# Performance work log

Hardware: AMD Instinct MI355X
Metric: run time of the kernel (lower is better)

The kernel has to match this reference:

```python
import jax, jax.numpy as jnp
import numpy as np

B, S, D, H, F, E, K = 2, 2048, 1024, 16, 4096, 8, 2
DK = D // H


def _ln(x, g, b, eps=1e-5):
    m = jnp.mean(x, axis=-1, keepdims=True)
    v = jnp.var(x, axis=-1, keepdims=True)
    return (x - m) * jax.lax.rsqrt(v + eps) * g + b


def _silu(x):
    return x * jax.nn.sigmoid(x)


def _gated_proj(x, w1, b1, w2, b2):
    # SiLU(x W1 + b1) * (x W2 + b2)
    return _silu(x @ w1 + b1) * (x @ w2 + b2)


def setup_inputs() -> dict:
    key = jax.random.key(0)
    ks = jax.random.split(key, 32)

    def n(k, shape, s=0.02):
        return jax.random.normal(k, shape, jnp.float32) * s

    inp = {
        "x": jax.random.normal(ks[0], (B, S, D), jnp.float32),
        "wq1": n(ks[1], (D, D)), "bq1": jnp.zeros((D,), jnp.float32),
        "wq2": n(ks[2], (D, D)), "bq2": jnp.zeros((D,), jnp.float32),
        "wk1": n(ks[3], (D, D)), "bk1": jnp.zeros((D,), jnp.float32),
        "wk2": n(ks[4], (D, D)), "bk2": jnp.zeros((D,), jnp.float32),
        "wv1": n(ks[5], (D, D)), "bv1": jnp.zeros((D,), jnp.float32),
        "wv2": n(ks[6], (D, D)), "bv2": jnp.zeros((D,), jnp.float32),
        "wo": n(ks[7], (D, D)), "bo": jnp.zeros((D,), jnp.float32),
        "ln1_g": jnp.ones((D,), jnp.float32), "ln1_b": jnp.zeros((D,), jnp.float32),
        "ln2_g": jnp.ones((D,), jnp.float32), "ln2_b": jnp.zeros((D,), jnp.float32),
        "gate_w": n(ks[8], (D, E)), "gate_b": jnp.zeros((E,), jnp.float32),
        "e_w1": n(ks[9], (E, D, F)), "e_b1": jnp.zeros((E, F), jnp.float32),
        "e_w2": n(ks[10], (E, F, D)), "e_b2": jnp.zeros((E, D), jnp.float32),
        "e_w3": n(ks[11], (E, D, F)), "e_b3": jnp.zeros((E, F), jnp.float32),
    }
    return inp


def _attention(x2, wq1, bq1, wq2, bq2, wk1, bk1, wk2, bk2,
               wv1, bv1, wv2, bv2, wo, bo, eps=1e-6):
    q = _gated_proj(x2, wq1, bq1, wq2, bq2).reshape(B, S, H, DK)
    k = _gated_proj(x2, wk1, bk1, wk2, bk2).reshape(B, S, H, DK)
    v = _gated_proj(x2, wv1, bv1, wv2, bv2).reshape(B, S, H, DK)
    phi_q = jax.nn.elu(q) + 1.0
    phi_k = jax.nn.elu(k) + 1.0
    # kv: [B,H,DK,DK] -- associative reordering of linear attention
    kv = jnp.einsum("bshd,bshe->bhde", phi_k, v)
    ksum = jnp.sum(phi_k, axis=1)  # [B,H,DK]
    qksum = jnp.einsum("bshd,bhd->bsh", phi_q, ksum)
    num = jnp.einsum("bshd,bhde->bshe", phi_q, kv)
    out = num / (qksum[..., None] + eps)  # [B,S,H,DK]
    return out.reshape(B, S, D) @ wo + bo


def _moe(x2, gate_w, gate_b, e_w1, e_b1, e_w2, e_b2, e_w3, e_b3):
    gate_probs = jax.nn.softmax(x2 @ gate_w + gate_b, axis=-1)  # [B,S,E]
    topv, topi = jax.lax.top_k(gate_probs, K)  # [B,S,K]
    topv = topv / (jnp.sum(topv, axis=-1, keepdims=True) + 1e-6)
    # combine weight per expert: [B,S,E]
    comb = jnp.sum(jax.nn.one_hot(topi, E, dtype=x2.dtype) * topv[..., None], axis=-2)
    out = jnp.zeros_like(x2)
    for e in range(E):  # small fixed expert count
        h = _silu(x2 @ e_w1[e] + e_b1[e]) * (x2 @ e_w3[e] + e_b3[e])
        out = out + (h @ e_w2[e] + e_b2[e]) * comb[..., e, None]
    return out


def reference(x, wq1, bq1, wq2, bq2, wk1, bk1, wk2, bk2, wv1, bv1, wv2, bv2,
              wo, bo, ln1_g, ln1_b, ln2_g, ln2_b, gate_w, gate_b,
              e_w1, e_b1, e_w2, e_b2, e_w3, e_b3):
    x2 = _ln(x, ln1_g, ln1_b)
    x = x + _attention(x2, wq1, bq1, wq2, bq2, wk1, bk1, wk2, bk2,
                       wv1, bv1, wv2, bv2, wo, bo)
    x2 = _ln(x, ln2_g, ln2_b)
    x = x + _moe(x2, gate_w, gate_b, e_w1, e_b1, e_w2, e_b2, e_w3, e_b3)
    return x
```

## Files before the change

kernel.cpp:

```cpp
#include <hip/hip_runtime.h>
#include <cstdint>
#include <cstddef>

typedef __bf16 bf16;
typedef bf16  bf16x8 __attribute__((ext_vector_type(8)));
typedef bf16  bf16x4 __attribute__((ext_vector_type(4)));
typedef float f32x4  __attribute__((ext_vector_type(4)));

#define B_ 2
#define S_ 2048
#define D_ 1024
#define H_ 16
#define F_ 4096
#define E_ 8
#define T_ (B_*S_)

__device__ __forceinline__ void gl16(const bf16* g, bf16* l) {
    __builtin_amdgcn_global_load_lds(
        (const __attribute__((address_space(1))) void*)g,
        (__attribute__((address_space(3))) void*)l, 16, 0, 0);
}

__global__ __launch_bounds__(256) void transpose_convert(const float* __restrict__ in,
                                                         bf16* __restrict__ out,
                                                         int R, int C) {
    __shared__ float tile[32][33];
    size_t mat = blockIdx.z;
    in  += mat * (size_t)R * C;
    out += mat * (size_t)R * C;
    int c0 = blockIdx.x * 32, r0 = blockIdx.y * 32;
    for (int i = threadIdx.y; i < 32; i += 8)
        tile[i][threadIdx.x] = in[(size_t)(r0 + i) * C + c0 + threadIdx.x];
    __syncthreads();
    for (int i = threadIdx.y; i < 32; i += 8)
        out[(size_t)(c0 + i) * R + r0 + threadIdx.x] = (bf16)tile[threadIdx.x][i];
}

__global__ __launch_bounds__(256) void ln_kernel(const float* __restrict__ xin,
                                                 const float* __restrict__ gam,
                                                 const float* __restrict__ bet,
                                                 bf16* __restrict__ obf,
                                                 float* __restrict__ of32) {
    int row = blockIdx.x, tid = threadIdx.x;
    const float4* xr = (const float4*)(xin + (size_t)row * D_);
    float4 v = xr[tid];
    float s  = v.x + v.y + v.z + v.w;
    float s2 = v.x*v.x + v.y*v.y + v.z*v.z + v.w*v.w;
    #pragma unroll
    for (int o = 1; o < 64; o <<= 1) { s += __shfl_xor(s, o); s2 += __shfl_xor(s2, o); }
    __shared__ float red[8];
    int wave = tid >> 6, lane = tid & 63;
    if (lane == 0) { red[wave] = s; red[4 + wave] = s2; }
    __syncthreads();
    s  = red[0] + red[1] + red[2] + red[3];
    s2 = red[4] + red[5] + red[6] + red[7];
    float m   = s * (1.0f / D_);
    float var = s2 * (1.0f / D_) - m * m;
    float rs  = rsqrtf(var + 1e-5f);
    float4 gv = ((const float4*)gam)[tid];
    float4 bv = ((const float4*)bet)[tid];
    float y0 = (v.x - m) * rs * gv.x + bv.x;
    float y1 = (v.y - m) * rs * gv.y + bv.y;
    float y2 = (v.z - m) * rs * gv.z + bv.z;
    float y3 = (v.w - m) * rs * gv.w + bv.w;
    bf16x4 ov; ov[0] = (bf16)y0; ov[1] = (bf16)y1; ov[2] = (bf16)y2; ov[3] = (bf16)y3;
    *(bf16x4*)(obf + (size_t)row * D_ + tid * 4) = ov;
    if (of32) {
        float4 o4; o4.x = y0; o4.y = y1; o4.z = y2; o4.w = y3;
        ((float4*)of32)[(size_t)row * (D_/4) + tid] = o4;
    }
}


template<int MODE>
__global__ __launch_bounds__(256) void gemm_dual128(const bf16* __restrict__ A,
                                                    const bf16* __restrict__ B1,
                                                    const bf16* __restrict__ B2,
                                                    const float* __restrict__ bias1,
                                                    const float* __restrict__ bias2,
                                                    float* __restrict__ out,
                                                    int N, int K) {
    __shared__ alignas(16) bf16 As [2][128 * 32];
    __shared__ alignas(16) bf16 B1s[2][64 * 32];
    __shared__ alignas(16) bf16 B2s[2][64 * 32];
    const int tid = threadIdx.x;
    const int wave = tid >> 6, lane = tid & 63;
    const int nb = blockIdx.x, mb = blockIdx.y;
    const int wr = (wave >> 1) * 64;
    const int wc = (wave & 1) * 32;
    const int fr = lane & 15, fk = (lane >> 4) * 8;
    const int srow = lane >> 2, scol = (lane & 3) * 8;
    const int co = wave * 512;
    const bf16* Ap0 = A  + (size_t)(mb * 128 + wave * 16 + srow) * K + scol;
    const bf16* Ap1 = A  + (size_t)(mb * 128 + (wave + 4) * 16 + srow) * K + scol;
    const bf16* B1p = B1 + (size_t)(nb * 64 + wave * 16 + srow) * K + scol;
    const bf16* B2p = B2 + (size_t)(nb * 64 + wave * 16 + srow) * K + scol;
    f32x4 acc1[4][2] = {};
    f32x4 acc2[4][2] = {};
    gl16(Ap0, &As[0][co]);
    gl16(Ap1, &As[0][co + 2048]);
    gl16(B1p, &B1s[0][co]);
    gl16(B2p, &B2s[0][co]);
    __syncthreads();
    int cur = 0;
    for (int k0 = 32; k0 < K; k0 += 32) {
        int nxt = cur ^ 1;
        gl16(Ap0 + k0, &As[nxt][co]);
        gl16(Ap1 + k0, &As[nxt][co + 2048]);
        gl16(B1p + k0, &B1s[nxt][co]);
        gl16(B2p + k0, &B2s[nxt][co]);
        bf16x8 af[4];
        #pragma unroll
        for (int mi = 0; mi < 4; mi++)
            af[mi] = *(const bf16x8*)&As[cur][(wr + mi * 16 + fr) * 32 + fk];
        #pragma unroll
        for (int ni = 0; ni < 2; ni++) {
            bf16x8 b1f = *(const bf16x8*)&B1s[cur][(wc + ni * 16 + fr) * 32 + fk];
            bf16x8 b2f = *(const bf16x8*)&B2s[cur][(wc + ni * 16 + fr) * 32 + fk];
            #pragma unroll
            for (int mi = 0; mi < 4; mi++) {
                acc1[mi][ni] = __builtin_amdgcn_mfma_f32_16x16x32_bf16(af[mi], b1f, acc1[mi][ni], 0, 0, 0);
                acc2[mi][ni] = __builtin_amdgcn_mfma_f32_16x16x32_bf16(af[mi], b2f, acc2[mi][ni], 0, 0, 0);
            }
        }
        __syncthreads();
        cur = nxt;
    }
    {
        bf16x8 af[4];
        #pragma unroll
        for (int mi = 0; mi < 4; mi++)
            af[mi] = *(const bf16x8*)&As[cur][(wr + mi * 16 + fr) * 32 + fk];
        #pragma unroll
        for (int ni = 0; ni < 2; ni++) {
            bf16x8 b1f = *(const bf16x8*)&B1s[cur][(wc + ni * 16 + fr) * 32 + fk];
            bf16x8 b2f = *(const bf16x8*)&B2s[cur][(wc + ni * 16 + fr) * 32 + fk];
            #pragma unroll
            for (int mi = 0; mi < 4; mi++) {
                acc1[mi][ni] = __builtin_amdgcn_mfma_f32_16x16x32_bf16(af[mi], b1f, acc1[mi][ni], 0, 0, 0);
                acc2[mi][ni] = __builtin_amdgcn_mfma_f32_16x16x32_bf16(af[mi], b2f, acc2[mi][ni], 0, 0, 0);
            }
        }
    }
    const int col = lane & 15, rowq = (lane >> 4) * 4;
    #pragma unroll
    for (int ni = 0; ni < 2; ni++) {
        int gn = nb * 64 + wc + ni * 16 + col;
        float bb1 = bias1[gn], bb2 = bias2[gn];
        #pragma unroll
        for (int mi = 0; mi < 4; mi++) {
            #pragma unroll
            for (int r = 0; r < 4; r++) {
                int gm = mb * 128 + wr + mi * 16 + rowq + r;
                float p1 = acc1[mi][ni][r] + bb1;
                float p2 = acc2[mi][ni][r] + bb2;
                float g = (p1 / (1.0f + expf(-p1))) * p2;
                size_t idx = (size_t)gm * N + gn;
                if (MODE == 0) {
                    float e = g > 0.0f ? g : expm1f(g);
                    out[idx] = e + 1.0f;
                } else {
                    out[idx] = g;
                }
            }
        }
    }
}

__global__ __launch_bounds__(256) void gemm_single128(const bf16* __restrict__ A,
                                                      const bf16* __restrict__ Bt,
                                                      float* __restrict__ out,
                                                      int N, int K) {
    __shared__ alignas(16) bf16 As[2][128 * 32];
    __shared__ alignas(16) bf16 Bs[2][128 * 32];
    const int tid = threadIdx.x;
    const int wave = tid >> 6, lane = tid & 63;
    const int nb = blockIdx.x, mb = blockIdx.y;
    const int wr = (wave >> 1) * 64, wc = (wave & 1) * 64;
    const int fr = lane & 15, fk = (lane >> 4) * 8;
    const int srow = lane >> 2, scol = (lane & 3) * 8;
    const int co = wave * 512;
    const bf16* Ap0 = A  + (size_t)(mb * 128 + wave * 16 + srow) * K + scol;
    const bf16* Ap1 = A  + (size_t)(mb * 128 + (wave + 4) * 16 + srow) * K + scol;
    const bf16* Bp0 = Bt + (size_t)(nb * 128 + wave * 16 + srow) * K + scol;
    const bf16* Bp1 = Bt + (size_t)(nb * 128 + (wave + 4) * 16 + srow) * K + scol;
    f32x4 acc[4][4] = {};
    gl16(Ap0, &As[0][co]);
    gl16(Ap1, &As[0][co + 2048]);
    gl16(Bp0, &Bs[0][co]);
    gl16(Bp1, &Bs[0][co + 2048]);
    __syncthreads();
    int cur = 0;
    for (int k0 = 32; k0 < K; k0 += 32) {
        int nxt = cur ^ 1;
        gl16(Ap0 + k0, &As[nxt][co]);
        gl16(Ap1 + k0, &As[nxt][co + 2048]);
        gl16(Bp0 + k0, &Bs[nxt][co]);
        gl16(Bp1 + k0, &Bs[nxt][co + 2048]);
        bf16x8 af[4], bf[4];
        #pragma unroll
        for (int mi = 0; mi < 4; mi++)
            af[mi] = *(const bf16x8*)&As[cur][(wr + mi * 16 + fr) * 32 + fk];
        #pragma unroll
        for (int ni = 0; ni < 4; ni++)
            bf[ni] = *(const bf16x8*)&Bs[cur][(wc + ni * 16 + fr) * 32 + fk];
        #pragma unroll
        for (int ni = 0; ni < 4; ni++)
            #pragma unroll
            for (int mi = 0; mi < 4; mi++)
                acc[mi][ni] = __builtin_amdgcn_mfma_f32_16x16x32_bf16(af[mi], bf[ni], acc[mi][ni], 0, 0, 0);
        __syncthreads();
        cur = nxt;
    }
    {
        bf16x8 af[4], bf[4];
        #pragma unroll
        for (int mi = 0; mi < 4; mi++)
            af[mi] = *(const bf16x8*)&As[cur][(wr + mi * 16 + fr) * 32 + fk];
        #pragma unroll
        for (int ni = 0; ni < 4; ni++)
            bf[ni] = *(const bf16x8*)&Bs[cur][(wc + ni * 16 + fr) * 32 + fk];
        #pragma unroll
        for (int ni = 0; ni < 4; ni++)
            #pragma unroll
            for (int mi = 0; mi < 4; mi++)
                acc[mi][ni] = __builtin_amdgcn_mfma_f32_16x16x32_bf16(af[mi], bf[ni], acc[mi][ni], 0, 0, 0);
    }
    const int col = lane & 15, rowq = (lane >> 4) * 4;
    #pragma unroll
    for (int ni = 0; ni < 4; ni++) {
        int gn = nb * 128 + wc + ni * 16 + col;
        #pragma unroll
        for (int mi = 0; mi < 4; mi++)
            #pragma unroll
            for (int r = 0; r < 4; r++) {
                int gm = mb * 128 + wr + mi * 16 + rowq + r;
                out[(size_t)gm * N + gn] = acc[mi][ni][r];
            }
    }
}

__global__ __launch_bounds__(256) void gemm_dual_moe128(const bf16* __restrict__ A,
                                                        const bf16* __restrict__ B1all,
                                                        const bf16* __restrict__ B2all,
                                                        const float* __restrict__ b1all,
                                                        const float* __restrict__ b2all,
                                                        const int* __restrict__ list,
                                                        const int* __restrict__ counts,
                                                        const int* __restrict__ ebase,
                                                        bf16* __restrict__ outAct,
                                                        int N, int K) {
    const int e = blockIdx.z;
    const int cnt = counts[e * 64];
    const int mb = blockIdx.y;
    if (mb * 128 >= cnt) return;
    __shared__ alignas(16) bf16 As [2][128 * 32];
    __shared__ alignas(16) bf16 B1s[2][64 * 32];
    __shared__ alignas(16) bf16 B2s[2][64 * 32];
    const bf16* B1 = B1all + (size_t)e * N * K;
    const bf16* B2 = B2all + (size_t)e * N * K;
    const float* bias1 = b1all + (size_t)e * N;
    const float* bias2 = b2all + (size_t)e * N;
    const int tid = threadIdx.x;
    const int wave = tid >> 6, lane = tid & 63;
    const int nb = blockIdx.x;
    const int wr = (wave >> 1) * 64, wc = (wave & 1) * 32;
    const int fr = lane & 15, fk = (lane >> 4) * 8;
    const int srow = lane >> 2, scol = (lane & 3) * 8;
    const int co = wave * 512;
    int gr0 = mb * 128 + wave * 16 + srow;
    int gr1 = mb * 128 + (wave + 4) * 16 + srow;
    int tok0 = list[e * T_ + (gr0 < cnt ? gr0 : cnt - 1)];
    int tok1 = list[e * T_ + (gr1 < cnt ? gr1 : cnt - 1)];
    const bf16* Ap0 = A  + (size_t)tok0 * K + scol;
    const bf16* Ap1 = A  + (size_t)tok1 * K + scol;
    const bf16* B1p = B1 + (size_t)(nb * 64 + wave * 16 + srow) * K + scol;
    const bf16* B2p = B2 + (size_t)(nb * 64 + wave * 16 + srow) * K + scol;
    f32x4 acc1[4][2] = {};
    f32x4 acc2[4][2] = {};
    gl16(Ap0, &As[0][co]);
    gl16(Ap1, &As[0][co + 2048]);
    gl16(B1p, &B1s[0][co]);
    gl16(B2p, &B2s[0][co]);
    __syncthreads();
    int cur = 0;
    for (int k0 = 32; k0 < K; k0 += 32) {
        int nxt = cur ^ 1;
        gl16(Ap0 + k0, &As[nxt][co]);
        gl16(Ap1 + k0, &As[nxt][co + 2048]);
        gl16(B1p + k0, &B1s[nxt][co]);
        gl16(B2p + k0, &B2s[nxt][co]);
        bf16x8 af[4];
        #pragma unroll
        for (int mi = 0; mi < 4; mi++)
            af[mi] = *(const bf16x8*)&As[cur][(wr + mi * 16 + fr) * 32 + fk];
        #pragma unroll
        for (int ni = 0; ni < 2; ni++) {
            bf16x8 b1f = *(const bf16x8*)&B1s[cur][(wc + ni * 16 + fr) * 32 + fk];
            bf16x8 b2f = *(const bf16x8*)&B2s[cur][(wc + ni * 16 + fr) * 32 + fk];
            #pragma unroll
            for (int mi = 0; mi < 4; mi++) {
                acc1[mi][ni] = __builtin_amdgcn_mfma_f32_16x16x32_bf16(af[mi], b1f, acc1[mi][ni], 0, 0, 0);
                acc2[mi][ni] = __builtin_amdgcn_mfma_f32_16x16x32_bf16(af[mi], b2f, acc2[mi][ni], 0, 0, 0);
            }
        }
        __syncthreads();
        cur = nxt;
    }
    {
        bf16x8 af[4];
        #pragma unroll
        for (int mi = 0; mi < 4; mi++)
            af[mi] = *(const bf16x8*)&As[cur][(wr + mi * 16 + fr) * 32 + fk];
        #pragma unroll
        for (int ni = 0; ni < 2; ni++) {
            bf16x8 b1f = *(const bf16x8*)&B1s[cur][(wc + ni * 16 + fr) * 32 + fk];
            bf16x8 b2f = *(const bf16x8*)&B2s[cur][(wc + ni * 16 + fr) * 32 + fk];
            #pragma unroll
            for (int mi = 0; mi < 4; mi++) {
                acc1[mi][ni] = __builtin_amdgcn_mfma_f32_16x16x32_bf16(af[mi], b1f, acc1[mi][ni], 0, 0, 0);
                acc2[mi][ni] = __builtin_amdgcn_mfma_f32_16x16x32_bf16(af[mi], b2f, acc2[mi][ni], 0, 0, 0);
            }
        }
    }
    const int col = lane & 15, rowq = (lane >> 4) * 4;
    const size_t rbase = (size_t)ebase[e] + mb * 128;
    #pragma unroll
    for (int ni = 0; ni < 2; ni++) {
        int gn = nb * 64 + wc + ni * 16 + col;
        float bb1 = bias1[gn], bb2 = bias2[gn];
        #pragma unroll
        for (int mi = 0; mi < 4; mi++)
            #pragma unroll
            for (int r = 0; r < 4; r++) {
                int lm = wr + mi * 16 + rowq + r;
                float p1 = acc1[mi][ni][r] + bb1;
                float p2 = acc2[mi][ni][r] + bb2;
                float g = (p1 / (1.0f + expf(-p1))) * p2;
                outAct[(rbase + lm) * N + gn] = (bf16)g;
            }
    }
}

__global__ __launch_bounds__(256) void gemm_down_moe128(const bf16* __restrict__ Act,
                                                        const bf16* __restrict__ Ball,
                                                        const float* __restrict__ ball,
                                                        const int* __restrict__ list,
                                                        const float* __restrict__ wgt,
                                                        const int* __restrict__ counts,
                                                        const int* __restrict__ ebase,
                                                        float* __restrict__ out,
                                                        int N, int K) {
    const int e = blockIdx.z;
    const int cnt = counts[e * 64];
    const int mb = blockIdx.y;
    if (mb * 128 >= cnt) return;
    __shared__ alignas(16) bf16 As[2][128 * 32];
    __shared__ alignas(16) bf16 Bs[2][128 * 32];
    const bf16* A  = Act + (size_t)ebase[e] * K;
    const bf16* Bt = Ball + (size_t)e * N * K;
    const float* bias = ball + (size_t)e * N;
    const int tid = threadIdx.x;
    const int wave = tid >> 6, lane = tid & 63;
    const int nb = blockIdx.x;
    const int wr = (wave >> 1) * 64, wc = (wave & 1) * 64;
    const int fr = lane & 15, fk = (lane >> 4) * 8;
    const int srow = lane >> 2, scol = (lane & 3) * 8;
    const int co = wave * 512;
    const bf16* Ap0 = A  + (size_t)(mb * 128 + wave * 16 + srow) * K + scol;
    const bf16* Ap1 = A  + (size_t)(mb * 128 + (wave + 4) * 16 + srow) * K + scol;
    const bf16* Bp0 = Bt + (size_t)(nb * 128 + wave * 16 + srow) * K + scol;
    const bf16* Bp1 = Bt + (size_t)(nb * 128 + (wave + 4) * 16 + srow) * K + scol;
    f32x4 acc[4][4] = {};
    gl16(Ap0, &As[0][co]);
    gl16(Ap1, &As[0][co + 2048]);
    gl16(Bp0, &Bs[0][co]);
    gl16(Bp1, &Bs[0][co + 2048]);
    __syncthreads();
    int cur = 0;
    for (int k0 = 32; k0 < K; k0 += 32) {
        int nxt = cur ^ 1;
        gl16(Ap0 + k0, &As[nxt][co]);
        gl16(Ap1 + k0, &As[nxt][co + 2048]);
        gl16(Bp0 + k0, &Bs[nxt][co]);
        gl16(Bp1 + k0, &Bs[nxt][co + 2048]);
        bf16x8 af[4], bf[4];
        #pragma unroll
        for (int mi = 0; mi < 4; mi++)
            af[mi] = *(const bf16x8*)&As[cur][(wr + mi * 16 + fr) * 32 + fk];
        #pragma unroll
        for (int ni = 0; ni < 4; ni++)
            bf[ni] = *(const bf16x8*)&Bs[cur][(wc + ni * 16 + fr) * 32 + fk];
        #pragma unroll
        for (int ni = 0; ni < 4; ni++)
            #pragma unroll
            for (int mi = 0; mi < 4; mi++)
                acc[mi][ni] = __builtin_amdgcn_mfma_f32_16x16x32_bf16(af[mi], bf[ni], acc[mi][ni], 0, 0, 0);
        __syncthreads();
        cur = nxt;
    }
    {
        bf16x8 af[4], bf[4];
        #pragma unroll
        for (int mi = 0; mi < 4; mi++)
            af[mi] = *(const bf16x8*)&As[cur][(wr + mi * 16 + fr) * 32 + fk];
        #pragma unroll
        for (int ni = 0; ni < 4; ni++)
            bf[ni] = *(const bf16x8*)&Bs[cur][(wc + ni * 16 + fr) * 32 + fk];
        #pragma unroll
        for (int ni = 0; ni < 4; ni++)
            #pragma unroll
            for (int mi = 0; mi < 4; mi++)
                acc[mi][ni] = __builtin_amdgcn_mfma_f32_16x16x32_bf16(af[mi], bf[ni], acc[mi][ni], 0, 0, 0);
    }
    const int col = lane & 15, rowq = (lane >> 4) * 4;
    #pragma unroll
    for (int ni = 0; ni < 4; ni++) {
        int gn = nb * 128 + wc + ni * 16 + col;
        float bb = bias[gn];
        #pragma unroll
        for (int mi = 0; mi < 4; mi++)
            #pragma unroll
            for (int r = 0; r < 4; r++) {
                int gm = mb * 128 + wr + mi * 16 + rowq + r;
                if (gm < cnt) {
                    int tok = list[e * T_ + gm];
                    float w = wgt[e * T_ + gm];
                    atomicAdd(&out[(size_t)tok * N + gn], (acc[mi][ni][r] + bb) * w);
                }
            }
    }
}

__global__ __launch_bounds__(256) void attn_kv_part(const float* __restrict__ phi_k,
                                                    const float* __restrict__ vv_g,
                                                    float* __restrict__ kvp,
                                                    float* __restrict__ ksp) {
    int bh = blockIdx.x;
    int chunk = blockIdx.y;
    int b = bh >> 4, h = bh & 15;
    __shared__ float pk[64][68];
    __shared__ float vv[64][68];
    int tid = threadIdx.x;
    int d0 = (tid >> 4) * 4;
    int e0 = (tid & 15) * 4;
    float acc[4][4] = {};
    float ks[4] = {};
    int sbeg = chunk * (S_ / 8);
    for (int s0 = sbeg; s0 < sbeg + S_ / 8; s0 += 64) {
        __syncthreads();
        for (int i = tid; i < 1024; i += 256) {
            int r = i >> 4, c4 = i & 15;
            size_t base = ((size_t)(b * S_ + s0 + r) * D_ + h * 64);
            ((float4*)&pk[r][0])[c4] = ((const float4*)(phi_k + base))[c4];
            ((float4*)&vv[r][0])[c4] = ((const float4*)(vv_g + base))[c4];
        }
        __syncthreads();
        for (int s = 0; s < 64; s++) {
            float a0 = pk[s][d0], a1 = pk[s][d0+1], a2 = pk[s][d0+2], a3 = pk[s][d0+3];
            float b0 = vv[s][e0], b1 = vv[s][e0+1], b2 = vv[s][e0+2], b3 = vv[s][e0+3];
            acc[0][0] += a0*b0; acc[0][1] += a0*b1; acc[0][2] += a0*b2; acc[0][3] += a0*b3;
            acc[1][0] += a1*b0; acc[1][1] += a1*b1; acc[1][2] += a1*b2; acc[1][3] += a1*b3;
            acc[2][0] += a2*b0; acc[2][1] += a2*b1; acc[2][2] += a2*b2; acc[2][3] += a2*b3;
            acc[3][0] += a3*b0; acc[3][1] += a3*b1; acc[3][2] += a3*b2; acc[3][3] += a3*b3;
            if ((tid & 15) == 0) { ks[0] += a0; ks[1] += a1; ks[2] += a2; ks[3] += a3; }
        }
    }
    float* kvo = kvp + ((size_t)bh * 8 + chunk) * 4096;
    for (int i = 0; i < 4; i++)
        for (int j = 0; j < 4; j++)
            kvo[(d0 + i) * 64 + e0 + j] = acc[i][j];
    if ((tid & 15) == 0)
        for (int i = 0; i < 4; i++) ksp[((size_t)bh * 8 + chunk) * 64 + d0 + i] = ks[i];
}

__global__ __launch_bounds__(256) void attn_kv_reduce(const float* __restrict__ kvp,
                                                      const float* __restrict__ ksp,
                                                      float* __restrict__ kv,
                                                      float* __restrict__ ksum) {
    int bh = blockIdx.x;
    int tid = threadIdx.x;
    #pragma unroll
    for (int i = 0; i < 4; i++) {
        int idx = i * 256 + tid;
        float4 s = {0, 0, 0, 0};
        #pragma unroll
        for (int c = 0; c < 8; c++) {
            float4 p = ((const float4*)(kvp + ((size_t)bh * 8 + c) * 4096))[idx];
            s.x += p.x; s.y += p.y; s.z += p.z; s.w += p.w;
        }
        ((float4*)(kv + (size_t)bh * 4096))[idx] = s;
    }
    if (tid < 64) {
        float s = 0;
        #pragma unroll
        for (int c = 0; c < 8; c++) s += ksp[((size_t)bh * 8 + c) * 64 + tid];
        ksum[bh * 64 + tid] = s;
    }
}

__global__ __launch_bounds__(256) void attn_num(const float* __restrict__ phi_q,
                                                const float* __restrict__ kv,
                                                const float* __restrict__ ksum,
                                                bf16* __restrict__ outb) {
    int bh = blockIdx.y;
    int b = bh >> 4, h = bh & 15;
    int s0 = blockIdx.x * 64;
    __shared__ float kvs[64][64];
    __shared__ float pqs[64][68];
    __shared__ float kss[64];
    int tid = threadIdx.x;
    const float* kvsrc = kv + (size_t)bh * 4096;
    for (int i = tid; i < 1024; i += 256) ((float4*)kvs)[i] = ((const float4*)kvsrc)[i];
    if (tid < 16) ((float4*)kss)[tid] = ((const float4*)(ksum + bh * 64))[tid];
    for (int i = tid; i < 1024; i += 256) {
        int r = i >> 4, c4 = i & 15;
        ((float4*)&pqs[r][0])[c4] =
            ((const float4*)(phi_q + ((size_t)(b * S_ + s0 + r) * D_ + h * 64)))[c4];
    }
    __syncthreads();
    int tok = tid >> 2;
    int e0  = (tid & 3) * 16;
    float acc[16] = {};
    float qk = 0.0f;
    for (int d = 0; d < 64; d++) {
        float pq = pqs[tok][d];
        qk += pq * kss[d];
        #pragma unroll
        for (int ei = 0; ei < 16; ei++) acc[ei] += pq * kvs[d][e0 + ei];
    }
    float inv = 1.0f / (qk + 1e-6f);
    int t = b * S_ + s0 + tok;
    bf16* op = outb + (size_t)t * D_ + h * 64 + e0;
    #pragma unroll
    for (int ei = 0; ei < 16; ei++) op[ei] = (bf16)(acc[ei] * inv);
}

__global__ __launch_bounds__(256) void residual_kernel(const float* __restrict__ x,
                                                       const float* __restrict__ prod,
                                                       const float* __restrict__ bo,
                                                       float* __restrict__ x1,
                                                       float* __restrict__ outp) {
    int i = blockIdx.x * 256 + threadIdx.x;
    float4 xv = ((const float4*)x)[i];
    float4 pv = ((const float4*)prod)[i];
    float4 bv = ((const float4*)bo)[i & 255];
    float4 r;
    r.x = xv.x + pv.x + bv.x; r.y = xv.y + pv.y + bv.y;
    r.z = xv.z + pv.z + bv.z; r.w = xv.w + pv.w + bv.w;
    ((float4*)x1)[i] = r;
    ((float4*)outp)[i] = r;
}

__global__ void zero_counts(int* counts) {
    counts[threadIdx.x] = 0;
}

__global__ void expert_bases(const int* __restrict__ counts, int* __restrict__ ebase) {
    if (threadIdx.x == 0) {
        int b = 0;
        #pragma unroll
        for (int e = 0; e < E_; e++) {
            ebase[e] = b;
            b += (counts[e * 64] + 127) & ~127;
        }
    }
}

__global__ __launch_bounds__(256) void gate_kernel(const float* __restrict__ x2f,
                                                   const float* __restrict__ gw,
                                                   const float* __restrict__ gb,
                                                   int* __restrict__ counts,
                                                   int* __restrict__ list,
                                                   float* __restrict__ wgt) {
    int tid = threadIdx.x;
    int wave = tid >> 6, lane = tid & 63;
    int t = blockIdx.x * 4 + wave;
    const float* xr = x2f + (size_t)t * D_;
    float le[8] = {};
    for (int i = 0; i < 16; i++) {
        int d = lane + i * 64;
        float xv = xr[d];
        const float4* g4 = (const float4*)(gw + (size_t)d * 8);
        float4 a = g4[0], b = g4[1];
        le[0] += xv * a.x; le[1] += xv * a.y; le[2] += xv * a.z; le[3] += xv * a.w;
        le[4] += xv * b.x; le[5] += xv * b.y; le[6] += xv * b.z; le[7] += xv * b.w;
    }
    #pragma unroll
    for (int o = 1; o < 64; o <<= 1)
        #pragma unroll
        for (int e = 0; e < 8; e++) le[e] += __shfl_xor(le[e], o);
    if (lane == 0) {
        float probs[8]; float mx = -1e30f;
        for (int e = 0; e < 8; e++) { le[e] += gb[e]; mx = fmaxf(mx, le[e]); }
        float s = 0.0f;
        for (int e = 0; e < 8; e++) { probs[e] = expf(le[e] - mx); s += probs[e]; }
        float invs = 1.0f / s;
        for (int e = 0; e < 8; e++) probs[e] *= invs;
        int i1 = 0; float v1 = probs[0];
        for (int e = 1; e < 8; e++) if (probs[e] > v1) { v1 = probs[e]; i1 = e; }
        int i2 = -1; float v2 = -1.0f;
        for (int e = 0; e < 8; e++) if (e != i1 && probs[e] > v2) { v2 = probs[e]; i2 = e; }
        float inv = 1.0f / (v1 + v2 + 1e-6f);
        int p1 = atomicAdd(&counts[i1 * 64], 1);
        list[i1 * T_ + p1] = t; wgt[i1 * T_ + p1] = v1 * inv;
        int p2 = atomicAdd(&counts[i2 * 64], 1);
        list[i2 * T_ + p2] = t; wgt[i2 * T_ + p2] = v2 * inv;
    }
}

extern "C" void kernel_launch(void* const* d_in, const int* in_sizes, int n_in,
                              void* d_out, int out_size, void* d_ws, size_t ws_size,
                              hipStream_t stream) {
    const float* x    = (const float*)d_in[0];
    const float* wq1  = (const float*)d_in[1];
    const float* bq1  = (const float*)d_in[2];
    const float* wq2  = (const float*)d_in[3];
    const float* bq2  = (const float*)d_in[4];
    const float* wk1  = (const float*)d_in[5];
    const float* bk1  = (const float*)d_in[6];
    const float* wk2  = (const float*)d_in[7];
    const float* bk2  = (const float*)d_in[8];
    const float* wv1  = (const float*)d_in[9];
    const float* bv1  = (const float*)d_in[10];
    const float* wv2  = (const float*)d_in[11];
    const float* bv2  = (const float*)d_in[12];
    const float* wo   = (const float*)d_in[13];
    const float* bo   = (const float*)d_in[14];
    const float* ln1g = (const float*)d_in[15];
    const float* ln1b = (const float*)d_in[16];
    const float* ln2g = (const float*)d_in[17];
    const float* ln2b = (const float*)d_in[18];
    const float* gw   = (const float*)d_in[19];
    const float* gb   = (const float*)d_in[20];
    const float* ew1  = (const float*)d_in[21];
    const float* eb1  = (const float*)d_in[22];
    const float* ew2  = (const float*)d_in[23];
    const float* eb2  = (const float*)d_in[24];
    const float* ew3  = (const float*)d_in[25];
    const float* eb3  = (const float*)d_in[26];
    float* out = (float*)d_out;

    char* wsb = (char*)d_ws;
    size_t off = 0;
    auto carve = [&](size_t bytes) -> char* {
        char* r = wsb + off;
        off = (off + bytes + 255) & ~(size_t)255;
        return r;
    };
    bf16* Wq1t = (bf16*)carve((size_t)D_ * D_ * 2);
    bf16* Wq2t = (bf16*)carve((size_t)D_ * D_ * 2);
    bf16* Wk1t = (bf16*)carve((size_t)D_ * D_ * 2);
    bf16* Wk2t = (bf16*)carve((size_t)D_ * D_ * 2);
    bf16* Wv1t = (bf16*)carve((size_t)D_ * D_ * 2);
    bf16* Wv2t = (bf16*)carve((size_t)D_ * D_ * 2);
    bf16* Wot  = (bf16*)carve((size_t)D_ * D_ * 2);
    bf16* We1t = (bf16*)carve((size_t)E_ * D_ * F_ * 2);
    bf16* We3t = (bf16*)carve((size_t)E_ * D_ * F_ * 2);
    bf16* We2t = (bf16*)carve((size_t)E_ * D_ * F_ * 2);
    bf16*  X2b  = (bf16*)carve((size_t)T_ * D_ * 2);
    float* PhiQ = (float*)carve((size_t)T_ * D_ * 4);
    float* PhiK = (float*)carve((size_t)T_ * D_ * 4);
    float* Vb   = (float*)carve((size_t)T_ * D_ * 4);
    float* KV   = (float*)carve((size_t)B_ * H_ * 64 * 64 * 4);
    float* KS   = (float*)carve((size_t)B_ * H_ * 64 * 4);
    float* KVp  = (float*)carve((size_t)B_ * H_ * 8 * 64 * 64 * 4);
    float* KSp  = (float*)carve((size_t)B_ * H_ * 8 * 64 * 4);
    bf16*  Attn = (bf16*)carve((size_t)T_ * D_ * 2);
    float* WoP  = (float*)carve((size_t)T_ * D_ * 4);
    float* X1   = (float*)carve((size_t)T_ * D_ * 4);
    bf16*  X2c  = (bf16*)carve((size_t)T_ * D_ * 2);
    int*   Cnt  = (int*)carve((size_t)E_ * 64 * 4);
    int*   List = (int*)carve((size_t)E_ * T_ * 4);
    float* Wgt  = (float*)carve((size_t)E_ * T_ * 4);
    int*   Ebase = (int*)carve((size_t)E_ * 4);
    bf16*  Act  = (bf16*)PhiQ;
    float* X2f  = WoP;

    dim3 tb32(32, 8);
    transpose_convert<<<dim3(32, 32, 1), tb32, 0, stream>>>(wq1, Wq1t, D_, D_);
    transpose_convert<<<dim3(32, 32, 1), tb32, 0, stream>>>(wq2, Wq2t, D_, D_);
    transpose_convert<<<dim3(32, 32, 1), tb32, 0, stream>>>(wk1, Wk1t, D_, D_);
    transpose_convert<<<dim3(32, 32, 1), tb32, 0, stream>>>(wk2, Wk2t, D_, D_);
    transpose_convert<<<dim3(32, 32, 1), tb32, 0, stream>>>(wv1, Wv1t, D_, D_);
    transpose_convert<<<dim3(32, 32, 1), tb32, 0, stream>>>(wv2, Wv2t, D_, D_);
    transpose_convert<<<dim3(32, 32, 1), tb32, 0, stream>>>(wo,  Wot,  D_, D_);
    transpose_convert<<<dim3(F_/32, D_/32, E_), tb32, 0, stream>>>(ew1, We1t, D_, F_);
    transpose_convert<<<dim3(F_/32, D_/32, E_), tb32, 0, stream>>>(ew3, We3t, D_, F_);
    transpose_convert<<<dim3(D_/32, F_/32, E_), tb32, 0, stream>>>(ew2, We2t, F_, D_);

    zero_counts<<<1, E_ * 64, 0, stream>>>(Cnt);

    ln_kernel<<<T_, 256, 0, stream>>>(x, ln1g, ln1b, X2b, nullptr);

    gemm_dual128<0><<<dim3(D_/64, T_/128), 256, 0, stream>>>(X2b, Wq1t, Wq2t, bq1, bq2, PhiQ, D_, D_);
    gemm_dual128<0><<<dim3(D_/64, T_/128), 256, 0, stream>>>(X2b, Wk1t, Wk2t, bk1, bk2, PhiK, D_, D_);
    gemm_dual128<1><<<dim3(D_/64, T_/128), 256, 0, stream>>>(X2b, Wv1t, Wv2t, bv1, bv2, Vb,   D_, D_);

    attn_kv_part<<<dim3(B_ * H_, 8), 256, 0, stream>>>(PhiK, Vb, KVp, KSp);
    attn_kv_reduce<<<B_ * H_, 256, 0, stream>>>(KVp, KSp, KV, KS);
    attn_num<<<dim3(S_/64, B_ * H_), 256, 0, stream>>>(PhiQ, KV, KS, Attn);

    gemm_single128<<<dim3(D_/128, T_/128), 256, 0, stream>>>(Attn, Wot, WoP, D_, D_);
    residual_kernel<<<T_ * D_ / 1024, 256, 0, stream>>>(x, WoP, bo, X1, out);

    ln_kernel<<<T_, 256, 0, stream>>>(X1, ln2g, ln2b, X2c, X2f);
    gate_kernel<<<T_ / 4, 256, 0, stream>>>(X2f, gw, gb, Cnt, List, Wgt);
    expert_bases<<<1, 64, 0, stream>>>(Cnt, Ebase);

    gemm_dual_moe128<<<dim3(F_/64, T_/128, E_), 256, 0, stream>>>(
        X2c, We1t, We3t, eb1, eb3, List, Cnt, Ebase, Act, F_, D_);
    gemm_down_moe128<<<dim3(D_/128, T_/128, E_), 256, 0, stream>>>(
        Act, We2t, eb2, List, Wgt, Cnt, Ebase, out, D_, F_);
}
```

Baseline: 1.159 ms.

## Triple-buffer GEMM K-loop with explicit waitcnt; vectorize weight transpose with swizzled LDS

All four GEMM kernels switch from double to triple-buffered LDS staging. Loads run two k-tiles ahead, and the full __syncthreads is replaced by s_waitcnt vmcnt(4) plus s_barrier, so global-to-LDS loads overlap more with MFMA work. The weight transpose/convert kernel now handles 256x64 tiles, reading with float4 and writing bf16x8 through an XOR-swizzled bf16 LDS buffer, which cuts per-element transactions. In exchange, LDS use per GEMM block rises by half, which may reduce occupancy, and the vmcnt counts must match exactly the four loads issued per stage.

```diff
diff --git a/kernel.cpp b/kernel.cpp
--- a/kernel.cpp
+++ b/kernel.cpp
@@ -24,16 +24,29 @@
 __global__ __launch_bounds__(256) void transpose_convert(const float* __restrict__ in,
                                                          bf16* __restrict__ out,
                                                          int R, int C) {
-    __shared__ float tile[32][33];
+    __shared__ bf16 tbuf[64 * 256];
     size_t mat = blockIdx.z;
     in  += mat * (size_t)R * C;
     out += mat * (size_t)R * C;
-    int c0 = blockIdx.x * 32, r0 = blockIdx.y * 32;
-    for (int i = threadIdx.y; i < 32; i += 8)
-        tile[i][threadIdx.x] = in[(size_t)(r0 + i) * C + c0 + threadIdx.x];
+    int c0 = blockIdx.x * 64, r0 = blockIdx.y * 256;
+    for (int i = threadIdx.x; i < 256 * 16; i += 256) {
+        int row = i >> 4, cb = (i & 15) * 4;
+        float4 v = *(const float4*)(in + (size_t)(r0 + row) * C + c0 + cb);
+        float vv[4] = {v.x, v.y, v.z, v.w};
+        #pragma unroll
+        for (int k = 0; k < 4; k++) {
+            int c = cb + k;
+            int key = ((c >> 2) & 7) << 3;
+            tbuf[c * 256 + (row ^ key)] = (bf16)vv[k];
+        }
+    }
     __syncthreads();
-    for (int i = threadIdx.y; i < 32; i += 8)
-        out[(size_t)(c0 + i) * R + r0 + threadIdx.x] = (bf16)tile[threadIdx.x][i];
+    for (int i = threadIdx.x; i < 64 * 32; i += 256) {
+        int c = i >> 5, r8 = (i & 31) * 8;
+        int key = ((c >> 2) & 7) << 3;
+        *(bf16x8*)(out + (size_t)(c0 + c) * R + r0 + r8) =
+            *(const bf16x8*)&tbuf[c * 256 + (r8 ^ key)];
+    }
 }
 
 __global__ __launch_bounds__(256) void ln_kernel(const float* __restrict__ xin,
@@ -80,14 +93,13 @@
                                                     const float* __restrict__ bias2,
                                                     float* __restrict__ out,
                                                     int N, int K) {
-    __shared__ alignas(16) bf16 As [2][128 * 32];
-    __shared__ alignas(16) bf16 B1s[2][64 * 32];
-    __shared__ alignas(16) bf16 B2s[2][64 * 32];
+    __shared__ alignas(16) bf16 As [3][128 * 32];
+    __shared__ alignas(16) bf16 B1s[3][64 * 32];
+    __shared__ alignas(16) bf16 B2s[3][64 * 32];
     const int tid = threadIdx.x;
     const int wave = tid >> 6, lane = tid & 63;
     const int nb = blockIdx.x, mb = blockIdx.y;
-    const int wr = (wave >> 1) * 64;
-    const int wc = (wave & 1) * 32;
+    const int wr = (wave >> 1) * 64, wc = (wave & 1) * 32;
     const int fr = lane & 15, fk = (lane >> 4) * 8;
     const int srow = lane >> 2, scol = (lane & 3) * 8;
     const int co = wave * 512;
@@ -97,51 +109,39 @@
     const bf16* B2p = B2 + (size_t)(nb * 64 + wave * 16 + srow) * K + scol;
     f32x4 acc1[4][2] = {};
     f32x4 acc2[4][2] = {};
-    gl16(Ap0, &As[0][co]);
-    gl16(Ap1, &As[0][co + 2048]);
-    gl16(B1p, &B1s[0][co]);
-    gl16(B2p, &B2s[0][co]);
-    __syncthreads();
-    int cur = 0;
-    for (int k0 = 32; k0 < K; k0 += 32) {
-        int nxt = cur ^ 1;
-        gl16(Ap0 + k0, &As[nxt][co]);
-        gl16(Ap1 + k0, &As[nxt][co + 2048]);
-        gl16(B1p + k0, &B1s[nxt][co]);
-        gl16(B2p + k0, &B2s[nxt][co]);
+    const int NT = K >> 5;
+#define STG_DU(t_, s_) { int k0_ = (t_) << 5; \
+        gl16(Ap0 + k0_, &As[s_][co]); \
+        gl16(Ap1 + k0_, &As[s_][co + 2048]); \
+        gl16(B1p + k0_, &B1s[s_][co]); \
+        gl16(B2p + k0_, &B2s[s_][co]); }
+    STG_DU(0, 0); STG_DU(1, 1);
+    asm volatile("s_waitcnt vmcnt(4)" ::: "memory");
+    __builtin_amdgcn_s_barrier();
+    for (int t = 0; t < NT; ++t) {
+        int s = t % 3;
+        if (t + 2 < NT) STG_DU(t + 2, (t + 2) % 3);
         bf16x8 af[4];
         #pragma unroll
         for (int mi = 0; mi < 4; mi++)
-            af[mi] = *(const bf16x8*)&As[cur][(wr + mi * 16 + fr) * 32 + fk];
+            af[mi] = *(const bf16x8*)&As[s][(wr + mi * 16 + fr) * 32 + fk];
         #pragma unroll
         for (int ni = 0; ni < 2; ni++) {
-            bf16x8 b1f = *(const bf16x8*)&B1s[cur][(wc + ni * 16 + fr) * 32 + fk];
-            bf16x8 b2f = *(const bf16x8*)&B2s[cur][(wc + ni * 16 + fr) * 32 + fk];
+            bf16x8 b1f = *(const bf16x8*)&B1s[s][(wc + ni * 16 + fr) * 32 + fk];
+            bf16x8 b2f = *(const bf16x8*)&B2s[s][(wc + ni * 16 + fr) * 32 + fk];
             #pragma unroll
             for (int mi = 0; mi < 4; mi++) {
                 acc1[mi][ni] = __builtin_amdgcn_mfma_f32_16x16x32_bf16(af[mi], b1f, acc1[mi][ni], 0, 0, 0);
                 acc2[mi][ni] = __builtin_amdgcn_mfma_f32_16x16x32_bf16(af[mi], b2f, acc2[mi][ni], 0, 0, 0);
             }
         }
-        __syncthreads();
-        cur = nxt;
-    }
-    {
-        bf16x8 af[4];
-        #pragma unroll
-        for (int mi = 0; mi < 4; mi++)
-            af[mi] = *(const bf16x8*)&As[cur][(wr + mi * 16 + fr) * 32 + fk];
-        #pragma unroll
-        for (int ni = 0; ni < 2; ni++) {
-            bf16x8 b1f = *(const bf16x8*)&B1s[cur][(wc + ni * 16 + fr) * 32 + fk];
-            bf16x8 b2f = *(const bf16x8*)&B2s[cur][(wc + ni * 16 + fr) * 32 + fk];
-            #pragma unroll
-            for (int mi = 0; mi < 4; mi++) {
-                acc1[mi][ni] = __builtin_amdgcn_mfma_f32_16x16x32_bf16(af[mi], b1f, acc1[mi][ni], 0, 0, 0);
-                acc2[mi][ni] = __builtin_amdgcn_mfma_f32_16x16x32_bf16(af[mi], b2f, acc2[mi][ni], 0, 0, 0);
-            }
-        }
-    }
+        if (t + 1 < NT) {
+            if (t + 2 < NT) asm volatile("s_waitcnt vmcnt(4) lgkmcnt(0)" ::: "memory");
+            else            asm volatile("s_waitcnt vmcnt(0) lgkmcnt(0)" ::: "memory");
+            __builtin_amdgcn_s_barrier();
+        }
+    }
+#undef STG_DU
     const int col = lane & 15, rowq = (lane >> 4) * 4;
     #pragma unroll
     for (int ni = 0; ni < 2; ni++) {
@@ -171,8 +171,8 @@
                                                       const bf16* __restrict__ Bt,
                                                       float* __restrict__ out,
                                                       int N, int K) {
-    __shared__ alignas(16) bf16 As[2][128 * 32];
-    __shared__ alignas(16) bf16 Bs[2][128 * 32];
+    __shared__ alignas(16) bf16 As[3][128 * 32];
+    __shared__ alignas(16) bf16 Bs[3][128 * 32];
     const int tid = threadIdx.x;
     const int wave = tid >> 6, lane = tid & 63;
     const int nb = blockIdx.x, mb = blockIdx.y;
@@ -185,47 +185,37 @@
     const bf16* Bp0 = Bt + (size_t)(nb * 128 + wave * 16 + srow) * K + scol;
     const bf16* Bp1 = Bt + (size_t)(nb * 128 + (wave + 4) * 16 + srow) * K + scol;
     f32x4 acc[4][4] = {};
-    gl16(Ap0, &As[0][co]);
-    gl16(Ap1, &As[0][co + 2048]);
-    gl16(Bp0, &Bs[0][co]);
-    gl16(Bp1, &Bs[0][co + 2048]);
-    __syncthreads();
-    int cur = 0;
-    for (int k0 = 32; k0 < K; k0 += 32) {
-        int nxt = cur ^ 1;
-        gl16(Ap0 + k0, &As[nxt][co]);
-        gl16(Ap1 + k0, &As[nxt][co + 2048]);
-        gl16(Bp0 + k0, &Bs[nxt][co]);
-        gl16(Bp1 + k0, &Bs[nxt][co + 2048]);
+    const int NT = K >> 5;
+#define STG_SG(t_, s_) { int k0_ = (t_) << 5; \
+        gl16(Ap0 + k0_, &As[s_][co]); \
+        gl16(Ap1 + k0_, &As[s_][co + 2048]); \
+        gl16(Bp0 + k0_, &Bs[s_][co]); \
+        gl16(Bp1 + k0_, &Bs[s_][co + 2048]); }
+    STG_SG(0, 0); STG_SG(1, 1);
+    asm volatile("s_waitcnt vmcnt(4)" ::: "memory");
+    __builtin_amdgcn_s_barrier();
+    for (int t = 0; t < NT; ++t) {
+        int s = t % 3;
+        if (t + 2 < NT) STG_SG(t + 2, (t + 2) % 3);
         bf16x8 af[4], bf[4];
         #pragma unroll
         for (int mi = 0; mi < 4; mi++)
-            af[mi] = *(const bf16x8*)&As[cur][(wr + mi * 16 + fr) * 32 + fk];
+            af[mi] = *(const bf16x8*)&As[s][(wr + mi * 16 + fr) * 32 + fk];
         #pragma unroll
         for (int ni = 0; ni < 4; ni++)
-            bf[ni] = *(const bf16x8*)&Bs[cur][(wc + ni * 16 + fr) * 32 + fk];
+            bf[ni] = *(const bf16x8*)&Bs[s][(wc + ni * 16 + fr) * 32 + fk];
         #pragma unroll
         for (int ni = 0; ni < 4; ni++)
             #pragma unroll
             for (int mi = 0; mi < 4; mi++)
                 acc[mi][ni] = __builtin_amdgcn_mfma_f32_16x16x32_bf16(af[mi], bf[ni], acc[mi][ni], 0, 0, 0);
-        __syncthreads();
-        cur = nxt;
-    }
-    {
-        bf16x8 af[4], bf[4];
-        #pragma unroll
-        for (int mi = 0; mi < 4; mi++)
-            af[mi] = *(const bf16x8*)&As[cur][(wr + mi * 16 + fr) * 32 + fk];
-        #pragma unroll
-        for (int ni = 0; ni < 4; ni++)
-            bf[ni] = *(const bf16x8*)&Bs[cur][(wc + ni * 16 + fr) * 32 + fk];
-        #pragma unroll
-        for (int ni = 0; ni < 4; ni++)
-            #pragma unroll
-            for (int mi = 0; mi < 4; mi++)
-                acc[mi][ni] = __builtin_amdgcn_mfma_f32_16x16x32_bf16(af[mi], bf[ni], acc[mi][ni], 0, 0, 0);
-    }
+        if (t + 1 < NT) {
+            if (t + 2 < NT) asm volatile("s_waitcnt vmcnt(4) lgkmcnt(0)" ::: "memory");
+            else            asm volatile("s_waitcnt vmcnt(0) lgkmcnt(0)" ::: "memory");
+            __builtin_amdgcn_s_barrier();
+        }
+    }
+#undef STG_SG
     const int col = lane & 15, rowq = (lane >> 4) * 4;
     #pragma unroll
     for (int ni = 0; ni < 4; ni++) {
@@ -254,9 +244,9 @@
     const int cnt = counts[e * 64];
     const int mb = blockIdx.y;
     if (mb * 128 >= cnt) return;
-    __shared__ alignas(16) bf16 As [2][128 * 32];
-    __shared__ alignas(16) bf16 B1s[2][64 * 32];
-    __shared__ alignas(16) bf16 B2s[2][64 * 32];
+    __shared__ alignas(16) bf16 As [3][128 * 32];
+    __shared__ alignas(16) bf16 B1s[3][64 * 32];
+    __shared__ alignas(16) bf16 B2s[3][64 * 32];
     const bf16* B1 = B1all + (size_t)e * N * K;
     const bf16* B2 = B2all + (size_t)e * N * K;
     const float* bias1 = b1all + (size_t)e * N;
@@ -278,51 +268,39 @@
     const bf16* B2p = B2 + (size_t)(nb * 64 + wave * 16 + srow) * K + scol;
     f32x4 acc1[4][2] = {};
     f32x4 acc2[4][2] = {};
-    gl16(Ap0, &As[0][co]);
-    gl16(Ap1, &As[0][co + 2048]);
-    gl16(B1p, &B1s[0][co]);
-    gl16(B2p, &B2s[0][co]);
-    __syncthreads();
-    int cur = 0;
-    for (int k0 = 32; k0 < K; k0 += 32) {
-        int nxt = cur ^ 1;
-        gl16(Ap0 + k0, &As[nxt][co]);
-        gl16(Ap1 + k0, &As[nxt][co + 2048]);
-        gl16(B1p + k0, &B1s[nxt][co]);
-        gl16(B2p + k0, &B2s[nxt][co]);
+    const int NT = K >> 5;
+#define STG_MU(t_, s_) { int k0_ = (t_) << 5; \
+        gl16(Ap0 + k0_, &As[s_][co]); \
+        gl16(Ap1 + k0_, &As[s_][co + 2048]); \
+        gl16(B1p + k0_, &B1s[s_][co]); \
+        gl16(B2p + k0_, &B2s[s_][co]); }
+    STG_MU(0, 0); STG_MU(1, 1);
+    asm volatile("s_waitcnt vmcnt(4)" ::: "memory");
+    __builtin_amdgcn_s_barrier();
+    for (int t = 0; t < NT; ++t) {
+        int s = t % 3;
+        if (t + 2 < NT) STG_MU(t + 2, (t + 2) % 3);
         bf16x8 af[4];
         #pragma unroll
         for (int mi = 0; mi < 4; mi++)
-            af[mi] = *(const bf16x8*)&As[cur][(wr + mi * 16 + fr) * 32 + fk];
+            af[mi] = *(const bf16x8*)&As[s][(wr + mi * 16 + fr) * 32 + fk];
         #pragma unroll
         for (int ni = 0; ni < 2; ni++) {
-            bf16x8 b1f = *(const bf16x8*)&B1s[cur][(wc + ni * 16 + fr) * 32 + fk];
-            bf16x8 b2f = *(const bf16x8*)&B2s[cur][(wc + ni * 16 + fr) * 32 + fk];
+            bf16x8 b1f = *(const bf16x8*)&B1s[s][(wc + ni * 16 + fr) * 32 + fk];
+            bf16x8 b2f = *(const bf16x8*)&B2s[s][(wc + ni * 16 + fr) * 32 + fk];
             #pragma unroll
             for (int mi = 0; mi < 4; mi++) {
                 acc1[mi][ni] = __builtin_amdgcn_mfma_f32_16x16x32_bf16(af[mi], b1f, acc1[mi][ni], 0, 0, 0);
                 acc2[mi][ni] = __builtin_amdgcn_mfma_f32_16x16x32_bf16(af[mi], b2f, acc2[mi][ni], 0, 0, 0);
             }
         }
-        __syncthreads();
-        cur = nxt;
-    }
-    {
-        bf16x8 af[4];
-        #pragma unroll
-        for (int mi = 0; mi < 4; mi++)
-            af[mi] = *(const bf16x8*)&As[cur][(wr + mi * 16 + fr) * 32 + fk];
-        #pragma unroll
-        for (int ni = 0; ni < 2; ni++) {
-            bf16x8 b1f = *(const bf16x8*)&B1s[cur][(wc + ni * 16 + fr) * 32 + fk];
-            bf16x8 b2f = *(const bf16x8*)&B2s[cur][(wc + ni * 16 + fr) * 32 + fk];
-            #pragma unroll
-            for (int mi = 0; mi < 4; mi++) {
-                acc1[mi][ni] = __builtin_amdgcn_mfma_f32_16x16x32_bf16(af[mi], b1f, acc1[mi][ni], 0, 0, 0);
-                acc2[mi][ni] = __builtin_amdgcn_mfma_f32_16x16x32_bf16(af[mi], b2f, acc2[mi][ni], 0, 0, 0);
-            }
-        }
-    }
+        if (t + 1 < NT) {
+            if (t + 2 < NT) asm volatile("s_waitcnt vmcnt(4) lgkmcnt(0)" ::: "memory");
+            else            asm volatile("s_waitcnt vmcnt(0) lgkmcnt(0)" ::: "memory");
+            __builtin_amdgcn_s_barrier();
+        }
+    }
+#undef STG_MU
     const int col = lane & 15, rowq = (lane >> 4) * 4;
     const size_t rbase = (size_t)ebase[e] + mb * 128;
     #pragma unroll
@@ -355,8 +333,8 @@
     const int cnt = counts[e * 64];
     const int mb = blockIdx.y;
     if (mb * 128 >= cnt) return;
-    __shared__ alignas(16) bf16 As[2][128 * 32];
-    __shared__ alignas(16) bf16 Bs[2][128 * 32];
+    __shared__ alignas(16) bf16 As[3][128 * 32];
+    __shared__ alignas(16) bf16 Bs[3][128 * 32];
     const bf16* A  = Act + (size_t)ebase[e] * K;
     const bf16* Bt = Ball + (size_t)e * N * K;
     const float* bias = ball + (size_t)e * N;
@@ -372,47 +350,37 @@
     const bf16* Bp0 = Bt + (size_t)(nb * 128 + wave * 16 + srow) * K + scol;
     const bf16* Bp1 = Bt + (size_t)(nb * 128 + (wave + 4) * 16 + srow) * K + scol;
     f32x4 acc[4][4] = {};
-    gl16(Ap0, &As[0][co]);
-    gl16(Ap1, &As[0][co + 2048]);
-    gl16(Bp0, &Bs[0][co]);
-    gl16(Bp1, &Bs[0][co + 2048]);
-    __syncthreads();
-    int cur = 0;
-    for (int k0 = 32; k0 < K; k0 += 32) {
-        int nxt = cur ^ 1;
-        gl16(Ap0 + k0, &As[nxt][co]);
-        gl16(Ap1 + k0, &As[nxt][co + 2048]);
-        gl16(Bp0 + k0, &Bs[nxt][co]);
-        gl16(Bp1 + k0, &Bs[nxt][co + 2048]);
+    const int NT = K >> 5;
+#define STG_MD(t_, s_) { int k0_ = (t_) << 5; \
+        gl16(Ap0 + k0_, &As[s_][co]); \
+        gl16(Ap1 + k0_, &As[s_][co + 2048]); \
+        gl16(Bp0 + k0_, &Bs[s_][co]); \
+        gl16(Bp1 + k0_, &Bs[s_][co + 2048]); }
+    STG_MD(0, 0); STG_MD(1, 1);
+    asm volatile("s_waitcnt vmcnt(4)" ::: "memory");
+    __builtin_amdgcn_s_barrier();
+    for (int t = 0; t < NT; ++t) {
+        int s = t % 3;
+        if (t + 2 < NT) STG_MD(t + 2, (t + 2) % 3);
         bf16x8 af[4], bf[4];
         #pragma unroll
         for (int mi = 0; mi < 4; mi++)
-            af[mi] = *(const bf16x8*)&As[cur][(wr + mi * 16 + fr) * 32 + fk];
+            af[mi] = *(const bf16x8*)&As[s][(wr + mi * 16 + fr) * 32 + fk];
         #pragma unroll
         for (int ni = 0; ni < 4; ni++)
-            bf[ni] = *(const bf16x8*)&Bs[cur][(wc + ni * 16 + fr) * 32 + fk];
+            bf[ni] = *(const bf16x8*)&Bs[s][(wc + ni * 16 + fr) * 32 + fk];
         #pragma unroll
         for (int ni = 0; ni < 4; ni++)
             #pragma unroll
             for (int mi = 0; mi < 4; mi++)
                 acc[mi][ni] = __builtin_amdgcn_mfma_f32_16x16x32_bf16(af[mi], bf[ni], acc[mi][ni], 0, 0, 0);
-        __syncthreads();
-        cur = nxt;
-    }
-    {
-        bf16x8 af[4], bf[4];
-        #pragma unroll
-        for (int mi = 0; mi < 4; mi++)
-            af[mi] = *(const bf16x8*)&As[cur][(wr + mi * 16 + fr) * 32 + fk];
-        #pragma unroll
-        for (int ni = 0; ni < 4; ni++)
-            bf[ni] = *(const bf16x8*)&Bs[cur][(wc + ni * 16 + fr) * 32 + fk];
-        #pragma unroll
-        for (int ni = 0; ni < 4; ni++)
-            #pragma unroll
-            for (int mi = 0; mi < 4; mi++)
-                acc[mi][ni] = __builtin_amdgcn_mfma_f32_16x16x32_bf16(af[mi], bf[ni], acc[mi][ni], 0, 0, 0);
-    }
+        if (t + 1 < NT) {
+            if (t + 2 < NT) asm volatile("s_waitcnt vmcnt(4) lgkmcnt(0)" ::: "memory");
+            else            asm volatile("s_waitcnt vmcnt(0) lgkmcnt(0)" ::: "memory");
+            __builtin_amdgcn_s_barrier();
+        }
+    }
+#undef STG_MD
     const int col = lane & 15, rowq = (lane >> 4) * 4;
     #pragma unroll
     for (int ni = 0; ni < 4; ni++) {
@@ -677,17 +645,16 @@
     bf16*  Act  = (bf16*)PhiQ;
     float* X2f  = WoP;
 
-    dim3 tb32(32, 8);
-    transpose_convert<<<dim3(32, 32, 1), tb32, 0, stream>>>(wq1, Wq1t, D_, D_);
-    transpose_convert<<<dim3(32, 32, 1), tb32, 0, stream>>>(wq2, Wq2t, D_, D_);
-    transpose_convert<<<dim3(32, 32, 1), tb32, 0, stream>>>(wk1, Wk1t, D_, D_);
-    transpose_convert<<<dim3(32, 32, 1), tb32, 0, stream>>>(wk2, Wk2t, D_, D_);
-    transpose_convert<<<dim3(32, 32, 1), tb32, 0, stream>>>(wv1, Wv1t, D_, D_);
-    transpose_convert<<<dim3(32, 32, 1), tb32, 0, stream>>>(wv2, Wv2t, D_, D_);
-    transpose_convert<<<dim3(32, 32, 1), tb32, 0, stream>>>(wo,  Wot,  D_, D_);
-    transpose_convert<<<dim3(F_/32, D_/32, E_), tb32, 0, stream>>>(ew1, We1t, D_, F_);
-    transpose_convert<<<dim3(F_/32, D_/32, E_), tb32, 0, stream>>>(ew3, We3t, D_, F_);
-    transpose_convert<<<dim3(D_/32, F_/32, E_), tb32, 0, stream>>>(ew2, We2t, F_, D_);
+    transpose_convert<<<dim3(D_/64, D_/256, 1), 256, 0, stream>>>(wq1, Wq1t, D_, D_);
+    transpose_convert<<<dim3(D_/64, D_/256, 1), 256, 0, stream>>>(wq2, Wq2t, D_, D_);
+    transpose_convert<<<dim3(D_/64, D_/256, 1), 256, 0, stream>>>(wk1, Wk1t, D_, D_);
+    transpose_convert<<<dim3(D_/64, D_/256, 1), 256, 0, stream>>>(wk2, Wk2t, D_, D_);
+    transpose_convert<<<dim3(D_/64, D_/256, 1), 256, 0, stream>>>(wv1, Wv1t, D_, D_);
+    transpose_convert<<<dim3(D_/64, D_/256, 1), 256, 0, stream>>>(wv2, Wv2t, D_, D_);
+    transpose_convert<<<dim3(D_/64, D_/256, 1), 256, 0, stream>>>(wo,  Wot,  D_, D_);
+    transpose_convert<<<dim3(F_/64, D_/256, E_), 256, 0, stream>>>(ew1, We1t, D_, F_);
+    transpose_convert<<<dim3(F_/64, D_/256, E_), 256, 0, stream>>>(ew3, We3t, D_, F_);
+    transpose_convert<<<dim3(D_/64, F_/256, E_), 256, 0, stream>>>(ew2, We2t, F_, D_);
 
     zero_counts<<<1, E_ * 64, 0, stream>>>(Cnt);
 
```

New measurement: 1.125 ms. -2.9%, faster.
